# Kernel optimization log

Hardware: AMD Instinct MI355X
Metric: run time of the kernel (lower is better)

The kernel has to match this reference:

```python
import jax, jax.numpy as jnp
import numpy as np

B, S, D, H = 8, 4096, 256, 256
MEM_COUNT = 3
FEAT = 7 * D + 2


def setup_inputs() -> dict:
    key = jax.random.key(0)
    ks = jax.random.split(key, 12)
    u = lambda k, shp: jax.random.uniform(k, shp, jnp.float32, -0.05, 0.05)
    return {
        "c": jax.random.normal(ks[0], (B, S, D), jnp.float32),
        "q": jax.random.normal(ks[1], (B, 1, D), jnp.float32),
        "len_c": jax.random.randint(ks[2], (B,), 1, S + 1),
        "att_weight": u(ks[3], (D, D)),
        "w1": u(ks[4], (H, FEAT)),
        "b1": jnp.zeros((H,), jnp.float32),
        "w2": u(ks[5], (1, H)),
        "b2": jnp.zeros((1,), jnp.float32),
        "w_ih": u(ks[6], (3 * D, D)),
        "w_hh": u(ks[7], (3 * D, D)),
        "b_ih": jnp.zeros((3 * D,), jnp.float32),
        "b_hh": jnp.zeros((3 * D,), jnp.float32),
    }


def gru_cell(x, h, w_ih, w_hh, b_ih, b_hh):
    # PyTorch GRUCell math
    gi = x @ w_ih.T + b_ih
    gh = h @ w_hh.T + b_hh
    i_r, i_z, i_n = jnp.split(gi, 3, axis=-1)
    h_r, h_z, h_n = jnp.split(gh, 3, axis=-1)
    r = jax.nn.sigmoid(i_r + h_r)
    z = jax.nn.sigmoid(i_z + h_z)
    n = jnp.tanh(i_n + r * h_n)
    return (1.0 - z) * n + z * h


def reference(c, q, len_c, att_weight, w1, b1, w2, b2, w_ih, w_hh, b_ih, b_hh):
    Bv, Sv, Dv = c.shape
    mask = jnp.arange(Sv)[None, :] < len_c[:, None]  # [B,S] valid positions
    cw = c @ att_weight                              # [B,S,D], reused each hop
    dot_q = jnp.einsum("bsd,bod->bso", cw, q)        # [B,S,1]
    m = q                                            # [B,1,D]
    atts = []
    for _ in range(MEM_COUNT):
        dot_m = jnp.einsum("bsd,bod->bso", cw, m)
        mb = jnp.broadcast_to(m, c.shape)
        qb = jnp.broadcast_to(q, c.shape)
        feat = jnp.concatenate(
            [c, mb, qb, c * q, c * m, jnp.abs(c - q), jnp.abs(c - m), dot_q, dot_m],
            axis=2,
        )                                            # [B,S,7D+2]
        h = jnp.tanh(feat @ w1.T + b1)               # [B,S,H]
        scores = (h @ w2.T + b2)[..., 0]             # [B,S]
        scores = jnp.where(mask, scores, -jnp.inf)
        att = jax.nn.softmax(scores, axis=1)
        att = jnp.where(mask, att, 0.0)[..., None]   # padded positions -> 0
        atts.append(att)
        e = (c * att).sum(axis=1)                    # [B,D]
        h_new = gru_cell(e, m[:, 0, :], w_ih, w_hh, b_ih, b_hh)
        m = h_new[:, None, :]
    return m[:, 0, :], jnp.stack(atts)
```

## Files before the change

### kernel.cpp

```cpp
#include <hip/hip_runtime.h>
#include <hip/hip_bf16.h>
#include <math.h>
#include <stdint.h>

#define B 8
#define S 4096
#define D 256
#define H 256
#define FEAT 1794
#define R (B*S)
#define DH (D*H)
#define NCH 64

typedef __bf16 bf16_t;
typedef __bf16 bf16x8 __attribute__((ext_vector_type(8)));
typedef float f32x4 __attribute__((ext_vector_type(4)));

__device__ __forceinline__ float waveReduceSum(float v) {
  #pragma unroll
  for (int off = 32; off; off >>= 1) v += __shfl_xor(v, off, 64);
  return v;
}

__global__ void k_init(const float* __restrict__ c, const float* __restrict__ q,
                       const float* __restrict__ w1, const float* __restrict__ A,
                       const int* __restrict__ len_c,
                       bf16_t* __restrict__ CBF, bf16_t* __restrict__ WAQ,
                       bf16_t* __restrict__ WAM, bf16_t* __restrict__ WAQM,
                       float* __restrict__ vq,
                       float* __restrict__ m0, float* __restrict__ epart,
                       float* __restrict__ ssum) {
  const int PREC_BLKS = R*D/2048;
  const int W_BLKS = DH/256;
  const int V_BLKS = B*64;
  const int blk = blockIdx.x;
  if (blk < PREC_BLKS) {
    const int row0 = blk * 8;
    const int b = row0 >> 12;
    if ((row0 & 4095) >= len_c[b]) return;
    int gid = blk * 256 + threadIdx.x;
    const float* cp = c + (size_t)gid*8;
    float cv[8];
    *(float4*)(cv)   = *(const float4*)(cp);
    *(float4*)(cv+4) = *(const float4*)(cp + 4);
    bf16x8 cb;
    #pragma unroll
    for (int i = 0; i < 8; i++) cb[i] = (bf16_t)cv[i];
    *(bf16x8*)(CBF + (size_t)gid*8) = cb;
  } else if (blk < PREC_BLKS + W_BLKS) {
    int idx = (blk - PREC_BLKS) * 256 + threadIdx.x;
    int h = idx >> 8, k = idx & 255;
    const float* w1h = w1 + (size_t)h * FEAT;
    float wq = w1h[5*D + k], wm = w1h[6*D + k];
    WAQ[idx]  = (bf16_t)wq;
    WAM[idx]  = (bf16_t)wm;
    WAQM[idx] = (bf16_t)(wq + wm);
  } else if (blk < PREC_BLKS + W_BLKS + V_BLKS) {
    const int blk2 = blk - PREC_BLKS - W_BLKS;
    const int b = blk2 >> 6;
    const int lane = threadIdx.x & 63, wave = threadIdx.x >> 6;
    const int t = (blk2 & 63)*4 + wave;
    const int l4 = lane * 4;
    float4 q4 = *(const float4*)(q + b*D + l4);
    float4 a4 = *(const float4*)(A + (size_t)t*D + l4);
    float s = a4.x*q4.x + a4.y*q4.y + a4.z*q4.z + a4.w*q4.w;
    s = waveReduceSum(s);
    if (lane == 0) vq[b*D + t] = s;
    if (threadIdx.x < 4) {
      const int tt = (blk2 & 63)*4 + threadIdx.x;
      m0[b*D + tt] = q[b*D + tt];
    }
  } else {
    const int b = blk - PREC_BLKS - W_BLKS - V_BLKS;
    const int ch0 = (len_c[b] + 63) >> 6;
    for (int ch = ch0; ch < NCH; ch++) {
      epart[(ch*B + b)*D + threadIdx.x] = 0.f;
      if (threadIdx.x == 0) ssum[ch*B + b] = 0.f;
    }
  }
}


__global__ void k_pm2(const float* __restrict__ A, const float* __restrict__ w1,
                      const float* __restrict__ b1, const float* __restrict__ q,
                      const float* __restrict__ min_,
                      float* __restrict__ vm, float* __restrict__ hb) {
  const int blk = blockIdx.x;
  const int b = blk >> 6;
  const int lane = threadIdx.x & 63, wave = threadIdx.x >> 6;
  const int t = (blk & 63)*4 + wave;
  const int l4 = lane * 4;
  float4 m4 = *(const float4*)(min_ + b*D + l4);
  float4 q4 = *(const float4*)(q + b*D + l4);
  float4 a4 = *(const float4*)(A + (size_t)t*D + l4);
  const float* w1r = w1 + (size_t)t*FEAT;
  float2 wm0 = *(const float2*)(w1r + D + l4);
  float2 wm1 = *(const float2*)(w1r + D + l4 + 2);
  float2 wq0 = *(const float2*)(w1r + 2*D + l4);
  float2 wq1 = *(const float2*)(w1r + 2*D + l4 + 2);
  float sv = a4.x*m4.x + a4.y*m4.y + a4.z*m4.z + a4.w*m4.w;
  float sh = m4.x*wm0.x + m4.y*wm0.y + m4.z*wm1.x + m4.w*wm1.y
           + q4.x*wq0.x + q4.y*wq0.y + q4.z*wq1.x + q4.w*wq1.y;
  sv = waveReduceSum(sv);
  sh = waveReduceSum(sh);
  if (lane == 0) { vm[b*D + t] = sv; hb[b*H + t] = b1[t] + sh; }
}

__global__ void k_comb(const float* __restrict__ w1, const float* __restrict__ q,
                       const float* __restrict__ min_,
                       const float* __restrict__ vq, const float* __restrict__ vm,
                       bf16_t* __restrict__ WCB) {
  int idx = blockIdx.x * 256 + threadIdx.x;
  int b = idx >> 16;
  int h = (idx >> 8) & 255;
  int k = idx & 255;
  const float* w1h = w1 + (size_t)h * FEAT;
  float v = w1h[k] + q[b*D + k]*w1h[3*D + k] + min_[b*D + k]*w1h[4*D + k]
          + vq[b*D + k]*w1h[7*D] + vm[b*D + k]*w1h[7*D + 1];
  WCB[idx] = (bf16_t)v;
}

template<int NS>
__global__ __launch_bounds__(512, 4) void k_score8(
    const bf16_t* __restrict__ CBF,
    const bf16_t* __restrict__ WCB, const bf16_t* __restrict__ WAQ,
    const bf16_t* __restrict__ WAM,
    const float* __restrict__ q, const float* __restrict__ min_,
    const int* __restrict__ len_c,
    const float* __restrict__ hb, const float* __restrict__ w2,
    const float* __restrict__ b2, float* __restrict__ esc,
    float* __restrict__ epart, float* __restrict__ ssum) {
  int b = 0, r0l = -1, accb = 0;
  const int flat = blockIdx.x;
  #pragma unroll
  for (int bb = 0; bb < 8; bb++) {
    const int nb = (len_c[bb] + 63) >> 6;
    if (r0l < 0 && flat < accb + nb) { b = bb; r0l = (flat - accb) << 6; }
    accb += nb;
  }
  if (r0l < 0) return;
  const int len = len_c[b];
  const int rowg = b*S + r0l;

  __shared__ char smem[49152];
  __shared__ float qshf[256], mshf[256];
  __shared__ float red[8][64];
  __shared__ float esh2[64];
  const int t = threadIdx.x;
  const int lane = t & 63, wave = t >> 6;
  const int lrow = lane & 15;
  const int lk = (lane >> 4) * 8;
  const int n0 = wave * 32;

  if (t < 256) { qshf[t] = q[b*D + t]; mshf[t] = min_[b*D + t]; }

  const int srow = t >> 3, sl = t & 7;
  const int sp = sl ^ (srow & 7);
  const int swbase = srow*128 + sp*16;
  const bf16_t* cgp = CBF + (size_t)(rowg + srow)*D + sl*8;

  const bf16_t* bptrC = WCB + (size_t)b*DH;
  const bf16_t* bptrQ = WAQ;
  const bf16_t* bptrM = WAM;

  f32x4 acc[4][2];
  #pragma unroll
  for (int mi = 0; mi < 4; mi++)
    #pragma unroll
    for (int ni = 0; ni < 2; ni++) acc[mi][ni] = (f32x4){0.f,0.f,0.f,0.f};

  bf16x8 breg[2][6];
  #define LOADB(ks) { \
    const int kelem = (ks)*32 + lk; \
    _Pragma("unroll") \
    for (int ni = 0; ni < 2; ni++) { \
      const size_t co = (size_t)(n0 + ni*16 + lrow) * D + kelem; \
      breg[(ks)&1][ni*3+0] = *(const bf16x8*)(bptrC + co); \
      breg[(ks)&1][ni*3+1] = *(const bf16x8*)(bptrQ + co); \
      if (NS == 3) breg[(ks)&1][ni*3+2] = *(const bf16x8*)(bptrM + co); \
    } }

  #define STAGESC(mc, cc, cr) { \
    const int kof = (mc)*128 + (cc)*64 + sl*8; \
    float qv_[8], mv_[8]; \
    *(float4*)(qv_)   = *(const float4*)(qshf + kof); \
    *(float4*)(qv_+4) = *(const float4*)(qshf + kof + 4); \
    *(float4*)(mv_)   = *(const float4*)(mshf + kof); \
    *(float4*)(mv_+4) = *(const float4*)(mshf + kof + 4); \
    bf16x8 aqv_, amv_; \
    _Pragma("unroll") \
    for (int i = 0; i < 8; i++) { \
      float cf_ = (float)(cr)[i]; \
      aqv_[i] = (bf16_t)fabsf(cf_ - qv_[i]); \
      if (NS == 3) amv_[i] = (bf16_t)fabsf(cf_ - mv_[i]); \
    } \
    char* lb_ = smem + (cc)*8192 + swbase; \
    *(bf16x8*)(lb_)         = (cr); \
    *(bf16x8*)(lb_ + 16384) = aqv_; \
    if (NS == 3) *(bf16x8*)(lb_ + 32768) = amv_; \
  }

  bf16x8 cA = *(const bf16x8*)(cgp);
  bf16x8 cB = *(const bf16x8*)(cgp + 64);
  LOADB(0);
  __syncthreads();
  STAGESC(0, 0, cA);
  STAGESC(0, 1, cB);
  cA = *(const bf16x8*)(cgp + 128);
  cB = *(const bf16x8*)(cgp + 192);
  __syncthreads();

  #pragma unroll
  for (int ks = 0; ks < 4; ks++) {
    LOADB(ks + 1);
    const int cc = ks >> 1, kk = ks & 1;
    const int p = ((kk << 2) + (lane >> 4)) ^ (lane & 7);
    const char* lb = smem + cc*8192;
    #pragma unroll
    for (int mi = 0; mi < 4; mi++) {
      const int ro = (mi*16 + lrow)*128 + p*16;
      bf16x8 ac = *(const bf16x8*)(lb + ro);
      bf16x8 aq = *(const bf16x8*)(lb + 16384 + ro);
      #pragma unroll
      for (int ni = 0; ni < 2; ni++) {
        acc[mi][ni] = __builtin_amdgcn_mfma_f32_16x16x32_bf16(ac, breg[ks&1][ni*3+0], acc[mi][ni], 0, 0, 0);
        acc[mi][ni] = __builtin_amdgcn_mfma_f32_16x16x32_bf16(aq, breg[ks&1][ni*3+1], acc[mi][ni], 0, 0, 0);
      }
      if (NS == 3) {
        bf16x8 am = *(const bf16x8*)(lb + 32768 + ro);
        #pragma unroll
        for (int ni = 0; ni < 2; ni++)
          acc[mi][ni] = __builtin_amdgcn_mfma_f32_16x16x32_bf16(am, breg[ks&1][ni*3+2], acc[mi][ni], 0, 0, 0);
      }
    }
  }
  __syncthreads();
  STAGESC(1, 0, cA);
  STAGESC(1, 1, cB);
  __syncthreads();

  #pragma unroll
  for (int ks = 4; ks < 8; ks++) {
    if (ks < 7) LOADB(ks + 1);
    const int cc = (ks >> 1) & 1, kk = ks & 1;
    const int p = ((kk << 2) + (lane >> 4)) ^ (lane & 7);
    const char* lb = smem + cc*8192;
    #pragma unroll
    for (int mi = 0; mi < 4; mi++) {
      const int ro = (mi*16 + lrow)*128 + p*16;
      bf16x8 ac = *(const bf16x8*)(lb + ro);
      bf16x8 aq = *(const bf16x8*)(lb + 16384 + ro);
      #pragma unroll
      for (int ni = 0; ni < 2; ni++) {
        acc[mi][ni] = __builtin_amdgcn_mfma_f32_16x16x32_bf16(ac, breg[ks&1][ni*3+0], acc[mi][ni], 0, 0, 0);
        acc[mi][ni] = __builtin_amdgcn_mfma_f32_16x16x32_bf16(aq, breg[ks&1][ni*3+1], acc[mi][ni], 0, 0, 0);
      }
      if (NS == 3) {
        bf16x8 am = *(const bf16x8*)(lb + 32768 + ro);
        #pragma unroll
        for (int ni = 0; ni < 2; ni++)
          acc[mi][ni] = __builtin_amdgcn_mfma_f32_16x16x32_bf16(am, breg[ks&1][ni*3+2], acc[mi][ni], 0, 0, 0);
      }
    }
  }

  float hbv[2], w2v[2];
  #pragma unroll
  for (int ni = 0; ni < 2; ni++) {
    const int col = n0 + ni*16 + lrow;
    hbv[ni] = hb[b*H + col];
    w2v[ni] = w2[col];
  }
  #pragma unroll
  for (int mi = 0; mi < 4; mi++) {
    #pragma unroll
    for (int j = 0; j < 4; j++) {
      float ps = 0.f;
      #pragma unroll
      for (int ni = 0; ni < 2; ni++) {
        float x = acc[mi][ni][j] + hbv[ni];
        float ex = __expf(2.f * x);
        float th = 1.f - 2.f * __builtin_amdgcn_rcpf(ex + 1.f);
        ps += th * w2v[ni];
      }
      ps += __shfl_xor(ps, 1, 64);
      ps += __shfl_xor(ps, 2, 64);
      ps += __shfl_xor(ps, 4, 64);
      ps += __shfl_xor(ps, 8, 64);
      if (lrow == 0) red[wave][mi*16 + (lane >> 4)*4 + j] = ps;
    }
  }
  __syncthreads();
  const int ch = r0l >> 6;
  if (t < 64) {
    float s = red[0][t] + red[1][t] + red[2][t] + red[3][t]
            + red[4][t] + red[5][t] + red[6][t] + red[7][t] + b2[0];
    float ev = (r0l + t < len) ? __expf(s) : 0.f;
    esc[b*S + r0l + t] = ev;
    esh2[t] = ev;
    float v = waveReduceSum(ev);
    if (t == 0) ssum[ch*B + b] = v;
  }
  __syncthreads();

  float* racc = (float*)smem;
  const int cg = t & 31, rg = t >> 5;
  float a8[8];
  #pragma unroll
  for (int i = 0; i < 8; i++) a8[i] = 0.f;
  #pragma unroll
  for (int j = 0; j < 4; j++) {
    const int sr = rg + j*16;
    const bf16x8 cv = *(const bf16x8*)(CBF + (size_t)(rowg + sr)*D + cg*8);
    const float a = esh2[sr];
    #pragma unroll
    for (int i = 0; i < 8; i++) a8[i] += a * (float)cv[i];
  }
  *(float4*)(&racc[rg*256 + cg*8])     = *(float4*)(a8);
  *(float4*)(&racc[rg*256 + cg*8 + 4]) = *(float4*)(a8 + 4);
  __syncthreads();
  if (t < 256) {
    float s2 = 0.f;
    #pragma unroll
    for (int g = 0; g < 16; g++) s2 += racc[g*256 + t];
    epart[(ch*B + b)*D + t] = s2;
  }
}

__global__ __launch_bounds__(256) void k_gru3(
    const float* __restrict__ wih, const float* __restrict__ whh,
    const float* __restrict__ bih, const float* __restrict__ bhh,
    const float* __restrict__ epart, const float* __restrict__ ssum,
    const float* __restrict__ esc, const int* __restrict__ len_c,
    const float* __restrict__ min_,
    float* __restrict__ att, float* __restrict__ mout,
    float* __restrict__ out, const int write_out) {
  const int blk = blockIdx.x;
  const int b = blk >> 4;
  const int p = blk & 15;
  const int t = threadIdx.x;
  const int lane = t & 63, wave = t >> 6;
  const int len = len_c[b];
  __shared__ float es[D], ms[D];
  __shared__ float Tsh;
  if (t < 64) {
    float v = waveReduceSum(ssum[t*B + b]);
    if (t == 0) Tsh = v;
  }
  float e = 0.f;
  #pragma unroll
  for (int ch = 0; ch < NCH; ch++) e += epart[(ch*B + b)*D + t];
  ms[t] = min_[b*D + t];
  __syncthreads();
  const float Tinv = 1.f / Tsh;
  es[t] = e * Tinv;
  const int sI = p*256 + t;
  att[b*S + sI] = (sI < len) ? esc[b*S + sI] * Tinv : 0.f;
  __syncthreads();
  const int t0 = p << 4;
  const int l4 = lane * 4;
  float4 e4 = *(const float4*)(es + l4);
  float4 m4 = *(const float4*)(ms + l4);
  #pragma unroll
  for (int tl = 0; tl < 4; tl++) {
    const int tt = t0 + wave*4 + tl;
    float g[6];
    #pragma unroll
    for (int gg = 0; gg < 3; gg++) {
      const int j = gg*D + tt;
      const float4 wi4 = *(const float4*)(wih + (size_t)j*D + l4);
      const float4 wh4 = *(const float4*)(whh + (size_t)j*D + l4);
      float gi = e4.x*wi4.x + e4.y*wi4.y + e4.z*wi4.z + e4.w*wi4.w;
      float gh = m4.x*wh4.x + m4.y*wh4.y + m4.z*wh4.z + m4.w*wh4.w;
      g[gg]   = waveReduceSum(gi);
      g[3+gg] = waveReduceSum(gh);
    }
    if (lane == 0) {
      const int j0 = tt, j1 = D + tt, j2 = 2*D + tt;
      float gir = g[0] + bih[j0], giz = g[1] + bih[j1], gin = g[2] + bih[j2];
      float ghr = g[3] + bhh[j0], ghz = g[4] + bhh[j1], ghn = g[5] + bhh[j2];
      float rr = 1.f / (1.f + __expf(-(gir + ghr)));
      float zz = 1.f / (1.f + __expf(-(giz + ghz)));
      float nn = tanhf(gin + rr * ghn);
      float mn = (1.f - zz)*nn + zz*ms[tt];
      mout[b*D + tt] = mn;
      if (write_out) out[b*D + tt] = mn;
    }
  }
}

extern "C" void kernel_launch(void* const* d_in, const int* in_sizes, int n_in,
                              void* d_out, int out_size, void* d_ws, size_t ws_size,
                              hipStream_t stream) {
  const float* c   = (const float*)d_in[0];
  const float* q   = (const float*)d_in[1];
  const int*   len = (const int*)d_in[2];
  const float* A   = (const float*)d_in[3];
  const float* w1  = (const float*)d_in[4];
  const float* b1  = (const float*)d_in[5];
  const float* w2  = (const float*)d_in[6];
  const float* b2  = (const float*)d_in[7];
  const float* wih = (const float*)d_in[8];
  const float* whh = (const float*)d_in[9];
  const float* bih = (const float*)d_in[10];
  const float* bhh = (const float*)d_in[11];
  float* out = (float*)d_out;

  bf16_t* WCB  = (bf16_t*)d_ws;
  bf16_t* WAQ  = WCB + (size_t)B*DH;
  bf16_t* WAM  = WAQ + DH;
  bf16_t* WAQM = WAM + DH;
  bf16_t* CBF  = WAQM + DH;
  float* fb = (float*)(CBF + (size_t)R*D);
  float* vq    = fb;
  float* vm    = vq + B*D;
  float* hb    = vm + B*D;
  float* m0    = hb + B*H;
  float* m1    = m0 + B*D;
  float* epart = m1 + B*D;
  float* esc   = epart + (size_t)NCH*B*D;
  float* ssum  = esc + R;

  k_init<<<R*D/2048 + DH/256 + B*64 + B, 256, 0, stream>>>(
      c, q, w1, A, len, CBF, WAQ, WAM, WAQM, vq, m0, epart, ssum);

  for (int it = 0; it < 3; ++it) {
    float* min_ = (it & 1) ? m1 : m0;
    float* mout = (it & 1) ? m0 : m1;
    k_pm2<<<B*64, 256, 0, stream>>>(A, w1, b1, q, min_, vm, hb);
    k_comb<<<B*DH/256, 256, 0, stream>>>(w1, q, min_, vq, vm, WCB);
    if (it == 0)
      k_score8<2><<<R/64, 512, 0, stream>>>(CBF, WCB, WAQM, WAM, q, min_, len, hb, w2, b2, esc, epart, ssum);
    else
      k_score8<3><<<R/64, 512, 0, stream>>>(CBF, WCB, WAQ, WAM, q, min_, len, hb, w2, b2, esc, epart, ssum);
    float* att = out + B*D + (size_t)it*R;
    k_gru3<<<B*16, 256, 0, stream>>>(wih, whh, bih, bhh, epart, ssum, esc, len, min_, att, mout, out, it == 2 ? 1 : 0);
  }
}
```

Measured before the change: 131.1 us.

## Fuse per-batch weight combination into score kernel and drop k_comb launches

```diff
diff --git a/kernel.cpp b/kernel.cpp
--- a/kernel.cpp
+++ b/kernel.cpp
@@ -24,10 +24,14 @@
 
 __global__ void k_init(const float* __restrict__ c, const float* __restrict__ q,
                        const float* __restrict__ w1, const float* __restrict__ A,
-                       const int* __restrict__ len_c,
-                       bf16_t* __restrict__ CBF, bf16_t* __restrict__ WAQ,
-                       bf16_t* __restrict__ WAM, bf16_t* __restrict__ WAQM,
-                       float* __restrict__ vq,
+                       const float* __restrict__ b1, const int* __restrict__ len_c,
+                       bf16_t* __restrict__ CBF,
+                       bf16_t* __restrict__ WC,  bf16_t* __restrict__ WCQ,
+                       bf16_t* __restrict__ WCM, bf16_t* __restrict__ WCQM,
+                       bf16_t* __restrict__ WAQ, bf16_t* __restrict__ WAM,
+                       bf16_t* __restrict__ WAQM,
+                       float* __restrict__ WDQ, float* __restrict__ WDM,
+                       float* __restrict__ vq, float* __restrict__ hb,
                        float* __restrict__ m0, float* __restrict__ epart,
                        float* __restrict__ ssum) {
   const int PREC_BLKS = R*D/2048;
@@ -51,10 +55,16 @@
     int idx = (blk - PREC_BLKS) * 256 + threadIdx.x;
     int h = idx >> 8, k = idx & 255;
     const float* w1h = w1 + (size_t)h * FEAT;
-    float wq = w1h[5*D + k], wm = w1h[6*D + k];
-    WAQ[idx]  = (bf16_t)wq;
-    WAM[idx]  = (bf16_t)wm;
-    WAQM[idx] = (bf16_t)(wq + wm);
+    float wc = w1h[k], wcq = w1h[3*D + k], wcm = w1h[4*D + k];
+    float waq = w1h[5*D + k], wam = w1h[6*D + k];
+    WC[idx]   = (bf16_t)wc;
+    WCQ[idx]  = (bf16_t)wcq;
+    WCM[idx]  = (bf16_t)wcm;
+    WCQM[idx] = (bf16_t)(wcq + wcm);
+    WAQ[idx]  = (bf16_t)waq;
+    WAM[idx]  = (bf16_t)wam;
+    WAQM[idx] = (bf16_t)(waq + wam);
+    if (k == 0) { WDQ[h] = w1h[7*D]; WDM[h] = w1h[7*D + 1]; }
   } else if (blk < PREC_BLKS + W_BLKS + V_BLKS) {
     const int blk2 = blk - PREC_BLKS - W_BLKS;
     const int b = blk2 >> 6;
@@ -66,6 +76,15 @@
     float s = a4.x*q4.x + a4.y*q4.y + a4.z*q4.z + a4.w*q4.w;
     s = waveReduceSum(s);
     if (lane == 0) vq[b*D + t] = s;
+    const float* w1r = w1 + (size_t)t*FEAT;
+    float2 wm0 = *(const float2*)(w1r + D + l4);
+    float2 wm1 = *(const float2*)(w1r + D + l4 + 2);
+    float2 wq0 = *(const float2*)(w1r + 2*D + l4);
+    float2 wq1 = *(const float2*)(w1r + 2*D + l4 + 2);
+    float sh = q4.x*(wm0.x + wq0.x) + q4.y*(wm0.y + wq0.y)
+             + q4.z*(wm1.x + wq1.x) + q4.w*(wm1.y + wq1.y);
+    sh = waveReduceSum(sh);
+    if (lane == 0) hb[b*H + t] = b1[t] + sh;
     if (threadIdx.x < 4) {
       const int tt = (blk2 & 63)*4 + threadIdx.x;
       m0[b*D + tt] = q[b*D + tt];
@@ -106,26 +125,15 @@
   if (lane == 0) { vm[b*D + t] = sv; hb[b*H + t] = b1[t] + sh; }
 }
 
-__global__ void k_comb(const float* __restrict__ w1, const float* __restrict__ q,
-                       const float* __restrict__ min_,
-                       const float* __restrict__ vq, const float* __restrict__ vm,
-                       bf16_t* __restrict__ WCB) {
-  int idx = blockIdx.x * 256 + threadIdx.x;
-  int b = idx >> 16;
-  int h = (idx >> 8) & 255;
-  int k = idx & 255;
-  const float* w1h = w1 + (size_t)h * FEAT;
-  float v = w1h[k] + q[b*D + k]*w1h[3*D + k] + min_[b*D + k]*w1h[4*D + k]
-          + vq[b*D + k]*w1h[7*D] + vm[b*D + k]*w1h[7*D + 1];
-  WCB[idx] = (bf16_t)v;
-}
-
 template<int NS>
-__global__ __launch_bounds__(512, 4) void k_score8(
+__global__ __launch_bounds__(512, 4) void k_score12(
     const bf16_t* __restrict__ CBF,
-    const bf16_t* __restrict__ WCB, const bf16_t* __restrict__ WAQ,
-    const bf16_t* __restrict__ WAM,
+    const bf16_t* __restrict__ WCp, const bf16_t* __restrict__ WCQp,
+    const bf16_t* __restrict__ WCMp,
+    const bf16_t* __restrict__ WAQp, const bf16_t* __restrict__ WAMp,
+    const float* __restrict__ WDQ, const float* __restrict__ WDM,
     const float* __restrict__ q, const float* __restrict__ min_,
+    const float* __restrict__ vqp, const float* __restrict__ vmp,
     const int* __restrict__ len_c,
     const float* __restrict__ hb, const float* __restrict__ w2,
     const float* __restrict__ b2, float* __restrict__ esc,
@@ -143,41 +151,63 @@
   const int rowg = b*S + r0l;
 
   __shared__ char smem[49152];
-  __shared__ float qshf[256], mshf[256];
+  __shared__ float qshf[256], mshf[256], vqshf[256], vmshf[256];
   __shared__ float red[8][64];
   __shared__ float esh2[64];
+  __shared__ float dqsh[64], dmsh[64];
   const int t = threadIdx.x;
   const int lane = t & 63, wave = t >> 6;
   const int lrow = lane & 15;
   const int lk = (lane >> 4) * 8;
   const int n0 = wave * 32;
 
-  if (t < 256) { qshf[t] = q[b*D + t]; mshf[t] = min_[b*D + t]; }
+  if (t < 256) {
+    qshf[t] = q[b*D + t];
+    mshf[t] = min_[b*D + t];
+    vqshf[t] = vqp[b*D + t];
+    if (NS == 3) vmshf[t] = vmp[b*D + t];
+  }
 
   const int srow = t >> 3, sl = t & 7;
   const int sp = sl ^ (srow & 7);
   const int swbase = srow*128 + sp*16;
   const bf16_t* cgp = CBF + (size_t)(rowg + srow)*D + sl*8;
 
-  const bf16_t* bptrC = WCB + (size_t)b*DH;
-  const bf16_t* bptrQ = WAQ;
-  const bf16_t* bptrM = WAM;
-
   f32x4 acc[4][2];
   #pragma unroll
   for (int mi = 0; mi < 4; mi++)
     #pragma unroll
     for (int ni = 0; ni < 2; ni++) acc[mi][ni] = (f32x4){0.f,0.f,0.f,0.f};
+
+  float dqa = 0.f, dma = 0.f;
 
   bf16x8 breg[2][6];
   #define LOADB(ks) { \
     const int kelem = (ks)*32 + lk; \
+    float qv8[8], mv8[8]; \
+    *(float4*)(qv8)   = *(const float4*)(qshf + kelem); \
+    *(float4*)(qv8+4) = *(const float4*)(qshf + kelem + 4); \
+    if (NS == 3) { \
+      *(float4*)(mv8)   = *(const float4*)(mshf + kelem); \
+      *(float4*)(mv8+4) = *(const float4*)(mshf + kelem + 4); \
+    } \
     _Pragma("unroll") \
     for (int ni = 0; ni < 2; ni++) { \
       const size_t co = (size_t)(n0 + ni*16 + lrow) * D + kelem; \
-      breg[(ks)&1][ni*3+0] = *(const bf16x8*)(bptrC + co); \
-      breg[(ks)&1][ni*3+1] = *(const bf16x8*)(bptrQ + co); \
-      if (NS == 3) breg[(ks)&1][ni*3+2] = *(const bf16x8*)(bptrM + co); \
+      bf16x8 wcv  = *(const bf16x8*)(WCp + co); \
+      bf16x8 wqv  = *(const bf16x8*)(WCQp + co); \
+      bf16x8 wmv; \
+      if (NS == 3) wmv = *(const bf16x8*)(WCMp + co); \
+      bf16x8 combv; \
+      _Pragma("unroll") \
+      for (int i = 0; i < 8; i++) { \
+        float v = (float)wcv[i] + qv8[i]*(float)wqv[i]; \
+        if (NS == 3) v += mv8[i]*(float)wmv[i]; \
+        combv[i] = (bf16_t)v; \
+      } \
+      breg[(ks)&1][ni*3+0] = combv; \
+      breg[(ks)&1][ni*3+1] = *(const bf16x8*)(WAQp + co); \
+      if (NS == 3) breg[(ks)&1][ni*3+2] = *(const bf16x8*)(WAMp + co); \
     } }
 
   #define STAGESC(mc, cc, cr) { \
@@ -185,14 +215,25 @@
     float qv_[8], mv_[8]; \
     *(float4*)(qv_)   = *(const float4*)(qshf + kof); \
     *(float4*)(qv_+4) = *(const float4*)(qshf + kof + 4); \
-    *(float4*)(mv_)   = *(const float4*)(mshf + kof); \
-    *(float4*)(mv_+4) = *(const float4*)(mshf + kof + 4); \
+    if (NS == 3) { \
+      *(float4*)(mv_)   = *(const float4*)(mshf + kof); \
+      *(float4*)(mv_+4) = *(const float4*)(mshf + kof + 4); \
+    } \
+    float vq_[8], vm_[8]; \
+    *(float4*)(vq_)   = *(const float4*)(vqshf + kof); \
+    *(float4*)(vq_+4) = *(const float4*)(vqshf + kof + 4); \
+    if (NS == 3) { \
+      *(float4*)(vm_)   = *(const float4*)(vmshf + kof); \
+      *(float4*)(vm_+4) = *(const float4*)(vmshf + kof + 4); \
+    } \
     bf16x8 aqv_, amv_; \
     _Pragma("unroll") \
     for (int i = 0; i < 8; i++) { \
       float cf_ = (float)(cr)[i]; \
       aqv_[i] = (bf16_t)fabsf(cf_ - qv_[i]); \
       if (NS == 3) amv_[i] = (bf16_t)fabsf(cf_ - mv_[i]); \
+      dqa += cf_ * vq_[i]; \
+      if (NS == 3) dma += cf_ * vm_[i]; \
     } \
     char* lb_ = smem + (cc)*8192 + swbase; \
     *(bf16x8*)(lb_)         = (cr); \
@@ -202,8 +243,8 @@
 
   bf16x8 cA = *(const bf16x8*)(cgp);
   bf16x8 cB = *(const bf16x8*)(cgp + 64);
+  __syncthreads();
   LOADB(0);
-  __syncthreads();
   STAGESC(0, 0, cA);
   STAGESC(0, 1, cB);
   cA = *(const bf16x8*)(cgp + 128);
@@ -237,6 +278,20 @@
   __syncthreads();
   STAGESC(1, 0, cA);
   STAGESC(1, 1, cB);
+  {
+    float dqv = dqa;
+    dqv += __shfl_xor(dqv, 1, 64);
+    dqv += __shfl_xor(dqv, 2, 64);
+    dqv += __shfl_xor(dqv, 4, 64);
+    if ((t & 7) == 0) dqsh[srow] = dqv;
+    if (NS == 3) {
+      float dmv = dma;
+      dmv += __shfl_xor(dmv, 1, 64);
+      dmv += __shfl_xor(dmv, 2, 64);
+      dmv += __shfl_xor(dmv, 4, 64);
+      if ((t & 7) == 0) dmsh[srow] = dmv;
+    }
+  }
   __syncthreads();
 
   #pragma unroll
@@ -264,21 +319,26 @@
     }
   }
 
-  float hbv[2], w2v[2];
+  float hbv[2], w2v[2], wdqv[2], wdmv[2];
   #pragma unroll
   for (int ni = 0; ni < 2; ni++) {
     const int col = n0 + ni*16 + lrow;
     hbv[ni] = hb[b*H + col];
     w2v[ni] = w2[col];
+    wdqv[ni] = WDQ[col];
+    wdmv[ni] = WDM[col];
   }
   #pragma unroll
   for (int mi = 0; mi < 4; mi++) {
     #pragma unroll
     for (int j = 0; j < 4; j++) {
+      const int row = mi*16 + (lane >> 4)*4 + j;
+      const float dqr = dqsh[row];
+      const float dmr = (NS == 3) ? dmsh[row] : dqr;
       float ps = 0.f;
       #pragma unroll
       for (int ni = 0; ni < 2; ni++) {
-        float x = acc[mi][ni][j] + hbv[ni];
+        float x = acc[mi][ni][j] + hbv[ni] + dqr*wdqv[ni] + dmr*wdmv[ni];
         float ex = __expf(2.f * x);
         float th = 1.f - 2.f * __builtin_amdgcn_rcpf(ex + 1.f);
         ps += th * w2v[ni];
@@ -287,7 +347,7 @@
       ps += __shfl_xor(ps, 2, 64);
       ps += __shfl_xor(ps, 4, 64);
       ps += __shfl_xor(ps, 8, 64);
-      if (lrow == 0) red[wave][mi*16 + (lane >> 4)*4 + j] = ps;
+      if (lrow == 0) red[wave][row] = ps;
     }
   }
   __syncthreads();
@@ -406,13 +466,18 @@
   const float* bhh = (const float*)d_in[11];
   float* out = (float*)d_out;
 
-  bf16_t* WCB  = (bf16_t*)d_ws;
-  bf16_t* WAQ  = WCB + (size_t)B*DH;
+  bf16_t* WC   = (bf16_t*)d_ws;
+  bf16_t* WCQ  = WC + DH;
+  bf16_t* WCM  = WCQ + DH;
+  bf16_t* WCQM = WCM + DH;
+  bf16_t* WAQ  = WCQM + DH;
   bf16_t* WAM  = WAQ + DH;
   bf16_t* WAQM = WAM + DH;
   bf16_t* CBF  = WAQM + DH;
   float* fb = (float*)(CBF + (size_t)R*D);
-  float* vq    = fb;
+  float* WDQ   = fb;
+  float* WDM   = WDQ + 256;
+  float* vq    = WDM + 256;
   float* vm    = vq + B*D;
   float* hb    = vm + B*D;
   float* m0    = hb + B*H;
@@ -422,17 +487,22 @@
   float* ssum  = esc + R;
 
   k_init<<<R*D/2048 + DH/256 + B*64 + B, 256, 0, stream>>>(
-      c, q, w1, A, len, CBF, WAQ, WAM, WAQM, vq, m0, epart, ssum);
+      c, q, w1, A, b1, len, CBF, WC, WCQ, WCM, WCQM, WAQ, WAM, WAQM,
+      WDQ, WDM, vq, hb, m0, epart, ssum);
 
   for (int it = 0; it < 3; ++it) {
     float* min_ = (it & 1) ? m1 : m0;
     float* mout = (it & 1) ? m0 : m1;
-    k_pm2<<<B*64, 256, 0, stream>>>(A, w1, b1, q, min_, vm, hb);
-    k_comb<<<B*DH/256, 256, 0, stream>>>(w1, q, min_, vq, vm, WCB);
-    if (it == 0)
-      k_score8<2><<<R/64, 512, 0, stream>>>(CBF, WCB, WAQM, WAM, q, min_, len, hb, w2, b2, esc, epart, ssum);
-    else
-      k_score8<3><<<R/64, 512, 0, stream>>>(CBF, WCB, WAQ, WAM, q, min_, len, hb, w2, b2, esc, epart, ssum);
+    if (it == 0) {
+      k_score12<2><<<R/64, 512, 0, stream>>>(
+          CBF, WC, WCQM, WCM, WAQM, WAM, WDQ, WDM,
+          q, min_, vq, vq, len, hb, w2, b2, esc, epart, ssum);
+    } else {
+      k_pm2<<<B*64, 256, 0, stream>>>(A, w1, b1, q, min_, vm, hb);
+      k_score12<3><<<R/64, 512, 0, stream>>>(
+          CBF, WC, WCQ, WCM, WAQ, WAM, WDQ, WDM,
+          q, min_, vq, vm, len, hb, w2, b2, esc, epart, ssum);
+    }
     float* att = out + B*D + (size_t)it*R;
     k_gru3<<<B*16, 256, 0, stream>>>(wih, whh, bih, bhh, epart, ssum, esc, len, min_, att, mout, out, it == 2 ? 1 : 0);
   }
```

Result: slower. 182.7 us (+39.3%).
